# Kernel tuning notes

Measured on AMD Instinct MI355X. Metric: run time of the kernel, lower is better.

Reference implementation:

```python
import jax, jax.numpy as jnp
import numpy as np

DIM = 2048
N_HEADS = 16
N_KV_HEADS = 4
HEAD_DIM = DIM // N_HEADS
N_REP = N_HEADS // N_KV_HEADS
ROPE_BASE = 10000.0


def _rope_cos_sin(seq_len, dtype):
    inv_freq = 1.0 / (ROPE_BASE ** (jnp.arange(0, HEAD_DIM, 2, dtype=jnp.float32) / HEAD_DIM))
    t = jnp.arange(seq_len, dtype=jnp.float32)
    freqs = jnp.einsum('s,d->sd', t, inv_freq)            # [S, head_dim/2]
    emb = jnp.concatenate([freqs, freqs], axis=-1)        # [S, head_dim]
    return jnp.cos(emb).astype(dtype), jnp.sin(emb).astype(dtype)


def _rotate_half(x):
    x1, x2 = jnp.split(x, 2, axis=-1)
    return jnp.concatenate([-x2, x1], axis=-1)


def _apply_rope(x, cos, sin):
    # x: [B, H, S, D]; cos/sin: [S, D]
    return x * cos[None, None, :, :] + _rotate_half(x) * sin[None, None, :, :]


def setup_inputs() -> dict:
    key = jax.random.key(0)
    ks = jax.random.split(key, 5)
    B, S = 2, 2048
    x = jax.random.normal(ks[0], (B, S, DIM), dtype=jnp.float32)
    sd = DIM ** -0.5
    wq = jax.random.normal(ks[1], (DIM, N_HEADS * HEAD_DIM), dtype=jnp.float32) * sd
    wk = jax.random.normal(ks[2], (DIM, N_KV_HEADS * HEAD_DIM), dtype=jnp.float32) * sd
    wv = jax.random.normal(ks[3], (DIM, N_KV_HEADS * HEAD_DIM), dtype=jnp.float32) * sd
    wo = jax.random.normal(ks[4], (DIM, DIM), dtype=jnp.float32) * sd
    return {'x': x, 'wq': wq, 'wk': wk, 'wv': wv, 'wo': wo}


def reference(x, wq, wk, wv, wo):
    B, S, _ = x.shape
    scale = HEAD_DIM ** -0.5
    q = (x @ wq).reshape(B, S, N_HEADS, HEAD_DIM).transpose(0, 2, 1, 3)      # [B,H,S,D]
    k = (x @ wk).reshape(B, S, N_KV_HEADS, HEAD_DIM).transpose(0, 2, 1, 3)   # [B,Hkv,S,D]
    v = (x @ wv).reshape(B, S, N_KV_HEADS, HEAD_DIM).transpose(0, 2, 1, 3)
    # repeat_interleave kv heads to match query heads
    k = jnp.repeat(k, N_REP, axis=1)                                          # [B,H,S,D]
    v = jnp.repeat(v, N_REP, axis=1)
    cos, sin = _rope_cos_sin(S, x.dtype)
    q = _apply_rope(q, cos, sin)
    k = _apply_rope(k, cos, sin)
    attn = jnp.einsum('bhqd,bhkd->bhqk', q, k) * scale
    causal = jnp.triu(jnp.ones((S, S), dtype=bool), k=1)
    attn = jnp.where(causal[None, None], -jnp.inf, attn)
    attn = jax.nn.softmax(attn.astype(jnp.float32), axis=-1).astype(q.dtype)
    out = jnp.einsum('bhqk,bhkd->bhqd', attn, v)
    out = out.transpose(0, 2, 1, 3).reshape(B, S, DIM)
    return out @ wo
```

## Files before the change

### kernel.cpp

```cpp
#include <hip/hip_runtime.h>
#include <hip/hip_bf16.h>

typedef __bf16 bf16_t;
typedef __attribute__((ext_vector_type(8))) __bf16 bf16x8;
typedef __attribute__((ext_vector_type(4))) float f32x4;

#define DIMN 2048
#define S_LEN 2048
#define B_SZ 2
#define NH 16
#define NKV 4
#define HD 128

__device__ __forceinline__ void gload_lds16(const void* g, void* l) {
    __builtin_amdgcn_global_load_lds((const __attribute__((address_space(1))) void*)g,
                                     (__attribute__((address_space(3))) void*)l, 16, 0, 0);
}

__global__ void cvt_kernel(const float* __restrict__ in, bf16_t* __restrict__ out, int n8) {
    int i = blockIdx.x * blockDim.x + threadIdx.x;
    if (i >= n8) return;
    const float4* p = (const float4*)in + (size_t)i * 2;
    float4 a = p[0], b = p[1];
    bf16x8 o;
    o[0] = (bf16_t)a.x; o[1] = (bf16_t)a.y; o[2] = (bf16_t)a.z; o[3] = (bf16_t)a.w;
    o[4] = (bf16_t)b.x; o[5] = (bf16_t)b.y; o[6] = (bf16_t)b.z; o[7] = (bf16_t)b.w;
    *((bf16x8*)out + i) = o;
}

__global__ void wt_transpose_kernel(const float* __restrict__ in, bf16_t* __restrict__ outp,
                                    int R, int C) {
    __shared__ bf16_t tile[32][33];
    int tx = threadIdx.x, ty = threadIdx.y;
    int r0 = blockIdx.y * 32, c0 = blockIdx.x * 32;
#pragma unroll
    for (int j = 0; j < 4; ++j)
        tile[ty + j * 8][tx] = (bf16_t)in[(size_t)(r0 + ty + j * 8) * C + c0 + tx];
    __syncthreads();
#pragma unroll
    for (int j = 0; j < 4; ++j)
        outp[(size_t)(c0 + ty + j * 8) * R + r0 + tx] = tile[tx][ty + j * 8];
}

__global__ void rope_table_kernel(float* __restrict__ cosT, float* __restrict__ sinT) {
    int idx = blockIdx.x * blockDim.x + threadIdx.x;
    int s = idx >> 6, j = idx & 63;
    float freq = powf(10000.f, -(float)j * (1.f / 64.f));
    float ang = (float)s * freq;
    cosT[idx] = cosf(ang);
    sinT[idx] = sinf(ang);
}

template<int HEADS>
__global__ void rope_apply_kernel(const bf16_t* __restrict__ in, bf16_t* __restrict__ outp,
                                  const float* __restrict__ cosT, const float* __restrict__ sinT,
                                  int in_stride) {
    int s = blockIdx.x, b = blockIdx.y;
    const int cols = HEADS * HD;
    int c0 = threadIdx.x * 8;
    if (c0 >= cols) return;
    int h = c0 >> 7, d = c0 & 127;
    int j = d & 63;
    const bf16_t* rowp = in + (size_t)(b * S_LEN + s) * in_stride;
    bf16x8 x = *(const bf16x8*)(rowp + c0);
    bf16x8 p = *(const bf16x8*)(rowp + (d < 64 ? c0 + 64 : c0 - 64));
    float sgn = (d < 64) ? -1.f : 1.f;
    bf16x8 o;
#pragma unroll
    for (int i = 0; i < 8; ++i) {
        float c = cosT[s * 64 + j + i];
        float sn = sinT[s * 64 + j + i];
        o[i] = (bf16_t)((float)x[i] * c + sgn * (float)p[i] * sn);
    }
    *(bf16x8*)(outp + ((size_t)(b * HEADS + h) * S_LEN + s) * HD + d) = o;
}

__global__ void vt_kernel(const bf16_t* __restrict__ vp, bf16_t* __restrict__ vt, int in_stride) {
    __shared__ bf16_t tile[32][33];
    int tx = threadIdx.x, ty = threadIdx.y;
    int s0 = blockIdx.x * 32;
    int d0 = blockIdx.y * 32;
    int bh = blockIdx.z;
    int b = bh >> 2, hkv = bh & 3;
#pragma unroll
    for (int j = 0; j < 4; ++j)
        tile[ty + j * 8][tx] =
            vp[(size_t)(b * S_LEN + s0 + ty + j * 8) * in_stride + hkv * HD + d0 + tx];
    __syncthreads();
#pragma unroll
    for (int j = 0; j < 4; ++j)
        vt[((size_t)(b * NKV + hkv) * HD + d0 + ty + j * 8) * S_LEN + s0 + tx] =
            tile[tx][ty + j * 8];
}

template<typename OT>
__global__ __launch_bounds__(256) void gemm_bt_kernel(const bf16_t* __restrict__ A,
                                                      const bf16_t* __restrict__ Bt,
                                                      OT* __restrict__ C,
                                                      int M, int N, int K) {
    __shared__ bf16_t As[128 * 32];
    __shared__ bf16_t Bs[128 * 32];
    int t = threadIdx.x;
    int w = t >> 6, l = t & 63;
    int wm = w >> 1, wn = w & 1;
    int m0 = blockIdx.y * 128, n0 = blockIdx.x * 128;
    int lr = l & 15, lg = l >> 4;
    f32x4 acc[4][4] = {};
    int row0 = t >> 2, cc0 = t & 3;
    int row1 = (256 + t) >> 2;
    for (int k0 = 0; k0 < K; k0 += 32) {
        gload_lds16(A + (size_t)(m0 + row0) * K + k0 + cc0 * 8, As + ((size_t)w * 64) * 8);
        gload_lds16(A + (size_t)(m0 + row1) * K + k0 + cc0 * 8, As + ((size_t)(256 + w * 64)) * 8);
        gload_lds16(Bt + (size_t)(n0 + row0) * K + k0 + cc0 * 8, Bs + ((size_t)w * 64) * 8);
        gload_lds16(Bt + (size_t)(n0 + row1) * K + k0 + cc0 * 8, Bs + ((size_t)(256 + w * 64)) * 8);
        __syncthreads();
        bf16x8 af[4], bfr[4];
#pragma unroll
        for (int mi = 0; mi < 4; ++mi)
            af[mi] = *(const bf16x8*)&As[(wm * 64 + mi * 16 + lr) * 32 + lg * 8];
#pragma unroll
        for (int ni = 0; ni < 4; ++ni)
            bfr[ni] = *(const bf16x8*)&Bs[(wn * 64 + ni * 16 + lr) * 32 + lg * 8];
#pragma unroll
        for (int mi = 0; mi < 4; ++mi)
#pragma unroll
            for (int ni = 0; ni < 4; ++ni)
                acc[mi][ni] = __builtin_amdgcn_mfma_f32_16x16x32_bf16(af[mi], bfr[ni],
                                                                     acc[mi][ni], 0, 0, 0);
        __syncthreads();
    }
#pragma unroll
    for (int mi = 0; mi < 4; ++mi) {
        int row = m0 + wm * 64 + mi * 16 + lg * 4;
#pragma unroll
        for (int ni = 0; ni < 4; ++ni) {
            int col = n0 + wn * 64 + ni * 16 + lr;
#pragma unroll
            for (int r = 0; r < 4; ++r) {
                float v = acc[mi][ni][r];
                C[(size_t)(row + r) * N + col] = (OT)v;
            }
        }
    }
}

__global__ __launch_bounds__(512) void attn_kernel(const bf16_t* __restrict__ qr,
                                                   const bf16_t* __restrict__ kr,
                                                   const bf16_t* __restrict__ vt,
                                                   bf16_t* __restrict__ outp) {
    __shared__ bf16_t Ks[2][64 * 128];
    __shared__ bf16_t Vs[2][128 * 64];
    __shared__ bf16_t p_lds[128][72];
    int t = threadIdx.x;
    int w = t >> 6, l = t & 63;
    int lr = l & 15, lg = l >> 4;
    int qt = (gridDim.x - 1) - blockIdx.x;
    int h = blockIdx.y, b = blockIdx.z;
    int hkv = h >> 2;
    const bf16_t* kbh = kr + (size_t)(b * NKV + hkv) * S_LEN * HD;
    const bf16_t* vbh = vt + (size_t)(b * NKV + hkv) * HD * S_LEN;
    int qrow0 = qt * 128 + w * 16;

    const bf16_t* qbase = qr + ((size_t)(b * NH + h) * S_LEN + qrow0 + lr) * HD;
    bf16x8 aq[4];
#pragma unroll
    for (int ks = 0; ks < 4; ++ks) aq[ks] = *(const bf16x8*)(qbase + ks * 32 + lg * 8);

    const char* ksrc[2];
    const char* vsrc[2];
    int ldsoff[2];
#pragma unroll
    for (int j = 0; j < 2; ++j) {
        int c = j * 512 + t;
        int o = c * 16;
        int aK = o ^ (((o >> 8) & 7) << 4);
        ksrc[j] = (const char*)kbh + (size_t)(aK >> 8) * 256 + (aK & 255);
        int aV = o ^ (((o >> 7) & 7) << 4);
        vsrc[j] = (const char*)vbh + (size_t)(aV >> 7) * (S_LEN * 2) + (aV & 127);
        ldsoff[j] = (j * 512 + w * 64) * 8;
    }

    f32x4 acc[8] = {};
    float l_r[4] = {0.f, 0.f, 0.f, 0.f};
    const float scale = 0.08838834764831845f;
    const float MMAX = 12.0f;
    int nt = 2 * qt + 2;

#pragma unroll
    for (int j = 0; j < 2; ++j) {
        gload_lds16(ksrc[j], &Ks[0][0] + ldsoff[j]);
        gload_lds16(vsrc[j], &Vs[0][0] + ldsoff[j]);
    }
    __syncthreads();

    int cur = 0;
    for (int kt = 0; kt < nt; ++kt) {
        if (kt + 1 < nt) {
#pragma unroll
            for (int j = 0; j < 2; ++j) {
                gload_lds16(ksrc[j] + (size_t)(kt + 1) * 16384, &Ks[cur ^ 1][0] + ldsoff[j]);
                gload_lds16(vsrc[j] + (size_t)(kt + 1) * 128, &Vs[cur ^ 1][0] + ldsoff[j]);
            }
        }
        bool active = (kt * 64 <= qrow0 + 15);
        if (active) {
            f32x4 sv[4] = {};
#pragma unroll
            for (int kn = 0; kn < 4; ++kn) {
                int krow = kn * 16 + lr;
#pragma unroll
                for (int ks = 0; ks < 4; ++ks) {
                    int a = krow * 256 + ks * 64 + lg * 16;
                    int phys = a ^ ((krow & 7) << 4);
                    bf16x8 bk = *(const bf16x8*)((const char*)&Ks[cur][0] + phys);
                    sv[kn] = __builtin_amdgcn_mfma_f32_16x16x32_bf16(aq[ks], bk, sv[kn], 0, 0, 0);
                }
            }
            bool needmask = (kt * 64 + 63 > qrow0);
            int qrow_lg = qrow0 + lg * 4;
#pragma unroll
            for (int kn = 0; kn < 4; ++kn) {
                int kg = kt * 64 + kn * 16 + lr;
#pragma unroll
                for (int r = 0; r < 4; ++r) {
                    float x = sv[kn][r] * scale - MMAX;
                    if (needmask && kg > qrow_lg + r) x = -1e30f;
                    float p = __expf(x);
                    sv[kn][r] = p;
                    l_r[r] += p;
                }
            }
#pragma unroll
            for (int kn = 0; kn < 4; ++kn)
#pragma unroll
                for (int r = 0; r < 4; ++r)
                    p_lds[w * 16 + lg * 4 + r][kn * 16 + lr] = (bf16_t)sv[kn][r];
#pragma unroll
            for (int ks2 = 0; ks2 < 2; ++ks2) {
                bf16x8 ap = *(const bf16x8*)&p_lds[w * 16 + lr][ks2 * 32 + lg * 8];
#pragma unroll
                for (int df = 0; df < 8; ++df) {
                    int vrow = df * 16 + lr;
                    int a = vrow * 128 + ks2 * 64 + lg * 16;
                    int phys = a ^ ((vrow & 7) << 4);
                    bf16x8 bv = *(const bf16x8*)((const char*)&Vs[cur][0] + phys);
                    acc[df] = __builtin_amdgcn_mfma_f32_16x16x32_bf16(ap, bv, acc[df], 0, 0, 0);
                }
            }
        }
        __syncthreads();
        cur ^= 1;
    }
    float lsum[4];
#pragma unroll
    for (int r = 0; r < 4; ++r) {
        float s = l_r[r];
#pragma unroll
        for (int off = 8; off >= 1; off >>= 1) s += __shfl_xor(s, off, 64);
        lsum[r] = s;
    }
#pragma unroll
    for (int df = 0; df < 8; ++df) {
        int col = h * HD + df * 16 + lr;
#pragma unroll
        for (int r = 0; r < 4; ++r) {
            float o = acc[df][r] / lsum[r];
            outp[(size_t)(b * S_LEN + qrow0 + lg * 4 + r) * DIMN + col] = (bf16_t)o;
        }
    }
}

extern "C" void kernel_launch(void* const* d_in, const int* in_sizes, int n_in,
                              void* d_out, int out_size, void* d_ws, size_t ws_size,
                              hipStream_t stream) {
    const float* x  = (const float*)d_in[0];
    const float* wq = (const float*)d_in[1];
    const float* wk = (const float*)d_in[2];
    const float* wv = (const float*)d_in[3];
    const float* wo = (const float*)d_in[4];
    float* outp = (float*)d_out;

    char* ws = (char*)d_ws;
    size_t off = 0;
    auto alloc = [&](size_t bytes) {
        char* p = ws + off;
        off += (bytes + 255) & ~255ull;
        return p;
    };
    const size_t MS = (size_t)B_SZ * S_LEN;
    const int NQKV = DIMN + 2 * 512;
    bf16_t* x_bf   = (bf16_t*)alloc(MS * DIMN * 2);
    bf16_t* wqkvt  = (bf16_t*)alloc((size_t)NQKV * DIMN * 2);
    bf16_t* wot    = (bf16_t*)alloc((size_t)DIMN * DIMN * 2);
    bf16_t* qkv    = (bf16_t*)alloc(MS * NQKV * 2);
    bf16_t* q_r    = (bf16_t*)alloc(MS * DIMN * 2);
    bf16_t* k_r    = (bf16_t*)alloc(MS * 512 * 2);
    bf16_t* v_t    = (bf16_t*)alloc(MS * 512 * 2);
    float*  cosT   = (float*)alloc((size_t)S_LEN * 64 * 4);
    float*  sinT   = (float*)alloc((size_t)S_LEN * 64 * 4);
    bf16_t* attn_o = x_bf;

    cvt_kernel<<<(int)(MS * DIMN / 8 / 256), 256, 0, stream>>>(x, x_bf, (int)(MS * DIMN / 8));
    wt_transpose_kernel<<<dim3(DIMN / 32, DIMN / 32), dim3(32, 8), 0, stream>>>(wq, wqkvt, DIMN, DIMN);
    wt_transpose_kernel<<<dim3(512 / 32, DIMN / 32), dim3(32, 8), 0, stream>>>(
        wk, wqkvt + (size_t)2048 * DIMN, DIMN, 512);
    wt_transpose_kernel<<<dim3(512 / 32, DIMN / 32), dim3(32, 8), 0, stream>>>(
        wv, wqkvt + (size_t)2560 * DIMN, DIMN, 512);
    wt_transpose_kernel<<<dim3(DIMN / 32, DIMN / 32), dim3(32, 8), 0, stream>>>(wo, wot, DIMN, DIMN);
    rope_table_kernel<<<S_LEN * 64 / 256, 256, 0, stream>>>(cosT, sinT);
    gemm_bt_kernel<bf16_t><<<dim3(NQKV / 128, MS / 128), 256, 0, stream>>>(x_bf, wqkvt, qkv,
                                                                           (int)MS, NQKV, DIMN);
    rope_apply_kernel<NH><<<dim3(S_LEN, B_SZ), 256, 0, stream>>>(qkv, q_r, cosT, sinT, NQKV);
    rope_apply_kernel<NKV><<<dim3(S_LEN, B_SZ), 64, 0, stream>>>(qkv + 2048, k_r, cosT, sinT, NQKV);
    vt_kernel<<<dim3(S_LEN / 32, HD / 32, B_SZ * NKV), dim3(32, 8), 0, stream>>>(qkv + 2560, v_t, NQKV);
    attn_kernel<<<dim3(S_LEN / 128, NH, B_SZ), 512, 0, stream>>>(q_r, k_r, v_t, attn_o);
    gemm_bt_kernel<float><<<dim3(DIMN / 128, MS / 128), 256, 0, stream>>>(attn_o, wot, outp,
                                                                          (int)MS, DIMN, DIMN);
}
```

Measured before the change: 384.8 us.

## Single-buffer attention K/V, raise occupancy, swizzle block order, add MFMA priority hints

The attention kernel drops K/V double buffering, which cuts shared memory so that, together with launch_bounds(512,4), more workgroups can be resident per CU. It also remaps blocks so heads sharing a KV head run close together, improving L2 reuse. The GEMM gets an XCD-style block-index swizzle, and both kernels wrap MFMA sections in s_setprio. The cost is that K/V loads are no longer overlapped with compute inside a block and an extra barrier is added each iteration, so the design relies on other resident blocks to hide the load latency.

```diff
diff --git a/kernel.cpp b/kernel.cpp
--- a/kernel.cpp
+++ b/kernel.cpp
@@ -103,7 +103,11 @@
     int t = threadIdx.x;
     int w = t >> 6, l = t & 63;
     int wm = w >> 1, wn = w & 1;
-    int m0 = blockIdx.y * 128, n0 = blockIdx.x * 128;
+    int nwg = gridDim.x * gridDim.y;
+    int flat = blockIdx.y * gridDim.x + blockIdx.x;
+    int swz = (flat & 7) * (nwg >> 3) + (flat >> 3);
+    int bx = swz % gridDim.x, by = swz / gridDim.x;
+    int m0 = by * 128, n0 = bx * 128;
     int lr = l & 15, lg = l >> 4;
     f32x4 acc[4][4] = {};
     int row0 = t >> 2, cc0 = t & 3;
@@ -121,12 +125,14 @@
 #pragma unroll
         for (int ni = 0; ni < 4; ++ni)
             bfr[ni] = *(const bf16x8*)&Bs[(wn * 64 + ni * 16 + lr) * 32 + lg * 8];
+        __builtin_amdgcn_s_setprio(1);
 #pragma unroll
         for (int mi = 0; mi < 4; ++mi)
 #pragma unroll
             for (int ni = 0; ni < 4; ++ni)
                 acc[mi][ni] = __builtin_amdgcn_mfma_f32_16x16x32_bf16(af[mi], bfr[ni],
                                                                      acc[mi][ni], 0, 0, 0);
+        __builtin_amdgcn_s_setprio(0);
         __syncthreads();
     }
 #pragma unroll
@@ -144,19 +150,21 @@
     }
 }
 
-__global__ __launch_bounds__(512) void attn_kernel(const bf16_t* __restrict__ qr,
-                                                   const bf16_t* __restrict__ kr,
-                                                   const bf16_t* __restrict__ vt,
-                                                   bf16_t* __restrict__ outp) {
-    __shared__ bf16_t Ks[2][64 * 128];
-    __shared__ bf16_t Vs[2][128 * 64];
+__global__ __launch_bounds__(512, 4) void attn_kernel(const bf16_t* __restrict__ qr,
+                                                      const bf16_t* __restrict__ kr,
+                                                      const bf16_t* __restrict__ vt,
+                                                      bf16_t* __restrict__ outp) {
+    __shared__ bf16_t Ks[64 * 128];
+    __shared__ bf16_t Vs[128 * 64];
     __shared__ bf16_t p_lds[128][72];
     int t = threadIdx.x;
     int w = t >> 6, l = t & 63;
     int lr = l & 15, lg = l >> 4;
-    int qt = (gridDim.x - 1) - blockIdx.x;
-    int h = blockIdx.y, b = blockIdx.z;
-    int hkv = h >> 2;
+    int flat = blockIdx.x + 16 * blockIdx.y + 256 * blockIdx.z;
+    int grp = flat & 7, rest = flat >> 3;
+    int b = grp >> 2, hkv = grp & 3;
+    int qt = 15 - (rest & 15);
+    int h = hkv * 4 + (rest >> 4);
     const bf16_t* kbh = kr + (size_t)(b * NKV + hkv) * S_LEN * HD;
     const bf16_t* vbh = vt + (size_t)(b * NKV + hkv) * HD * S_LEN;
     int qrow0 = qt * 128 + w * 16;
@@ -188,23 +196,16 @@
 
 #pragma unroll
     for (int j = 0; j < 2; ++j) {
-        gload_lds16(ksrc[j], &Ks[0][0] + ldsoff[j]);
-        gload_lds16(vsrc[j], &Vs[0][0] + ldsoff[j]);
+        gload_lds16(ksrc[j], &Ks[0] + ldsoff[j]);
+        gload_lds16(vsrc[j], &Vs[0] + ldsoff[j]);
     }
     __syncthreads();
 
-    int cur = 0;
     for (int kt = 0; kt < nt; ++kt) {
-        if (kt + 1 < nt) {
-#pragma unroll
-            for (int j = 0; j < 2; ++j) {
-                gload_lds16(ksrc[j] + (size_t)(kt + 1) * 16384, &Ks[cur ^ 1][0] + ldsoff[j]);
-                gload_lds16(vsrc[j] + (size_t)(kt + 1) * 128, &Vs[cur ^ 1][0] + ldsoff[j]);
-            }
-        }
         bool active = (kt * 64 <= qrow0 + 15);
         if (active) {
             f32x4 sv[4] = {};
+            __builtin_amdgcn_s_setprio(1);
 #pragma unroll
             for (int kn = 0; kn < 4; ++kn) {
                 int krow = kn * 16 + lr;
@@ -212,10 +213,11 @@
                 for (int ks = 0; ks < 4; ++ks) {
                     int a = krow * 256 + ks * 64 + lg * 16;
                     int phys = a ^ ((krow & 7) << 4);
-                    bf16x8 bk = *(const bf16x8*)((const char*)&Ks[cur][0] + phys);
+                    bf16x8 bk = *(const bf16x8*)((const char*)&Ks[0] + phys);
                     sv[kn] = __builtin_amdgcn_mfma_f32_16x16x32_bf16(aq[ks], bk, sv[kn], 0, 0, 0);
                 }
             }
+            __builtin_amdgcn_s_setprio(0);
             bool needmask = (kt * 64 + 63 > qrow0);
             int qrow_lg = qrow0 + lg * 4;
 #pragma unroll
@@ -235,6 +237,7 @@
 #pragma unroll
                 for (int r = 0; r < 4; ++r)
                     p_lds[w * 16 + lg * 4 + r][kn * 16 + lr] = (bf16_t)sv[kn][r];
+            __builtin_amdgcn_s_setprio(1);
 #pragma unroll
             for (int ks2 = 0; ks2 < 2; ++ks2) {
                 bf16x8 ap = *(const bf16x8*)&p_lds[w * 16 + lr][ks2 * 32 + lg * 8];
@@ -243,13 +246,21 @@
                     int vrow = df * 16 + lr;
                     int a = vrow * 128 + ks2 * 64 + lg * 16;
                     int phys = a ^ ((vrow & 7) << 4);
-                    bf16x8 bv = *(const bf16x8*)((const char*)&Vs[cur][0] + phys);
+                    bf16x8 bv = *(const bf16x8*)((const char*)&Vs[0] + phys);
                     acc[df] = __builtin_amdgcn_mfma_f32_16x16x32_bf16(ap, bv, acc[df], 0, 0, 0);
                 }
             }
+            __builtin_amdgcn_s_setprio(0);
         }
         __syncthreads();
-        cur ^= 1;
+        if (kt + 1 < nt) {
+#pragma unroll
+            for (int j = 0; j < 2; ++j) {
+                gload_lds16(ksrc[j] + (size_t)(kt + 1) * 16384, &Ks[0] + ldsoff[j]);
+                gload_lds16(vsrc[j] + (size_t)(kt + 1) * 128, &Vs[0] + ldsoff[j]);
+            }
+            __syncthreads();
+        }
     }
     float lsum[4];
 #pragma unroll
```

Measured after the change: 344.0 us. 10.6% less time.
